# Kernel optimization log

Hardware: AMD Instinct MI355X
Metric: run time of the kernel (lower is better)

Reference implementation:

```python
import jax, jax.numpy as jnp
import numpy as np

# GeoTempScheduler default: init_temp=0.1, gamma=0.9, patience=1; at step 0 -> temp = 0.1
TEMP = 0.1

R, K, D, DLOW, B = 8, 10, 256, 10, 4096


def setup_inputs() -> dict:
    key = jax.random.key(0)
    k1, k2 = jax.random.split(key)
    x = jax.random.normal(k1, (B, D), dtype=jnp.float32)
    # reset_parameters: Us ~ N(0, 0.1/sqrt(D))
    Us = jax.random.normal(k2, (R, K, D, DLOW), dtype=jnp.float32) * (0.1 / np.sqrt(D))
    return {"x": x, "Us": Us}


def reference(x, Us):
    # encode: project data onto each (replicate, cluster) subspace basis
    # z: (r, k, B, d)
    z = jnp.einsum('bD,rkDd->rkbd', x, Us)
    # decode: x_ = z @ Us^T  -> (r, k, B, D)
    x_ = jnp.einsum('rkbd,rkDd->rkbD', z, Us)
    # l2-squared reconstruction loss, (r, k, B) -> permuted to (B, r, k)
    loss = 0.5 * jnp.sum((x_ - x) ** 2, axis=-1)
    assign_obj = jnp.transpose(loss, (2, 0, 1))  # (B, r, k)
    # set_assign uses detached objective (loss.data): temperature-scaled soft assignment
    c = jax.nn.softmax(-jax.lax.stop_gradient(assign_obj) / TEMP, axis=2)  # (B, r, k)
    # x_ * c.permute(1,2,0).unsqueeze(3), summed over clusters -> (r, B, D)
    out = jnp.einsum('rkbD,brk->rbD', x_, c)
    return out
```

## Files before the change

### kernel.cpp

```cpp
#include <hip/hip_runtime.h>
#include <math.h>

typedef unsigned short ushort_t;
typedef unsigned int uint32_tt;
typedef __attribute__((ext_vector_type(8))) short bf16x8;
typedef __attribute__((ext_vector_type(4))) float f32x4;

#define NR   8
#define NK   10
#define ND   256
#define NDL  10
#define NB   4096
#define NN   100
#define NP   112
#define NP2  128

#define WS_GP   0
#define WS_XB   32768
#define WS_U1   (32768 + 2097152)
#define WS_U2   (WS_U1 + 458752)
#define WS_NEED (WS_U2 + 524288)

__device__ __forceinline__ ushort_t f2bf(float f) {
    uint32_tt u = __float_as_uint(f);
    u = (u + 0x7FFF + ((u >> 16) & 1)) >> 16;
    return (ushort_t)u;
}

__global__ __launch_bounds__(256) void prep_kernel(const float* __restrict__ x,
                                                   const float* __restrict__ Us,
                                                   char* __restrict__ ws) {
    __shared__ float lu[ND * NDL];
    const int bid = blockIdx.x, tid = threadIdx.x;

    if (bid >= 80) {
        ushort_t* xb = (ushort_t*)(ws + WS_XB);
        const int base = (bid - 80) * 1024;
        #pragma unroll
        for (int v = 0; v < 4; ++v) {
            int i = base + v * 256 + tid;
            float4 vv = ((const float4*)x)[i];
            uint32_tt p0 = (uint32_tt)f2bf(vv.x) | ((uint32_tt)f2bf(vv.y) << 16);
            uint32_tt p1 = (uint32_tt)f2bf(vv.z) | ((uint32_tt)f2bf(vv.w) << 16);
            ((uint2*)xb)[i] = make_uint2(p0, p1);
        }
        return;
    }

    const int rk = bid;
    const int r  = rk / NK, k = rk - r * NK;
    const float* U = Us + (size_t)rk * ND * NDL;
    for (int i = tid; i < 640; i += 256)
        ((float4*)lu)[i] = ((const float4*)U)[i];
    __syncthreads();

    float* Gp = (float*)(ws + WS_GP);
    if (tid < NDL * NDL) {
        int d1 = tid / NDL, d2 = tid - d1 * NDL;
        float acc = 0.f;
        #pragma unroll 8
        for (int Di = 0; Di < ND; ++Di)
            acc += lu[Di * NDL + d1] * lu[Di * NDL + d2];
        Gp[(size_t)rk * 100 + tid] = (d1 == d2 ? 10.0f : 0.0f) - 5.0f * acc;
    }

    ushort_t* u1 = (ushort_t*)(ws + WS_U1);
    for (int p = tid; p < ND * NDL; p += 256) {
        int d = p >> 8, D = p & 255;
        u1[((size_t)r * NP + k * NDL + d) * ND + D] = f2bf(lu[D * NDL + d]);
    }

    ushort_t* u2 = (ushort_t*)(ws + WS_U2);
    {
        int D = tid;
        uint32_tt* dst = (uint32_tt*)(u2 + ((size_t)r * ND + D) * NP2 + k * NDL);
        const float* src = lu + D * NDL;
        #pragma unroll
        for (int j = 0; j < 5; ++j)
            dst[j] = (uint32_tt)f2bf(src[2 * j]) | ((uint32_tt)f2bf(src[2 * j + 1]) << 16);
    }

    if (k == NK - 1) {
        for (int p = tid; p < 12 * ND; p += 256) {
            int n = p >> 8, D = p & 255;
            u1[((size_t)r * NP + 100 + n) * ND + D] = 0;
        }
        uint32_tt* u2u = (uint32_tt*)u2;
        #pragma unroll
        for (int j = 0; j < 14; ++j)
            u2u[((size_t)r * ND + tid) * (NP2 / 2) + 50 + j] = 0;
    }
}

__global__ __launch_bounds__(256, 2) void ksub_mfma8(const char* __restrict__ ws,
                                                     float* __restrict__ out) {
    __shared__ __align__(16) char smem[37280];
    float*    zbuf = (float*)smem;
    ushort_t* wTb  = (ushort_t*)smem;
    float*    ot   = (float*)smem;
    float*    gp   = (float*)(smem + 33280);

    const int tid  = threadIdx.x;
    const int w    = tid >> 6;
    const int lane = tid & 63;
    const int c    = lane & 15;
    const int q    = lane >> 4;
    const int bid  = blockIdx.x;
    const int xcd  = bid & 7;
    const int idx  = bid >> 3;
    const int r    = idx & 7;
    const int b0   = (xcd * 16 + (idx >> 3)) * 32;
    const int bloc = (w & 1) * 16 + c;
    const int pair = w >> 1;

    const ushort_t* xb  = (const ushort_t*)(ws + WS_XB) + (size_t)(b0 + bloc) * ND + q * 8;
    const ushort_t* u1g = (const ushort_t*)(ws + WS_U1) + (size_t)r * NP * ND + c * ND + q * 8;
    const ushort_t* u2g = (const ushort_t*)(ws + WS_U2) + (size_t)r * ND * NP2 + c * NP2 + q * 8;
    const float*    gpg = (const float*)(ws + WS_GP) + (size_t)r * 1000;

    for (int i = tid; i < 1000; i += 256) gp[i] = gpg[i];

    bf16x8 xfr[8];
    #pragma unroll
    for (int Dc = 0; Dc < 8; ++Dc)
        xfr[Dc] = *(const bf16x8*)(xb + Dc * 32);

    f32x4 acc1[4];
    #pragma unroll
    for (int t = 0; t < 4; ++t) acc1[t] = (f32x4){0.f, 0.f, 0.f, 0.f};

    #pragma unroll
    for (int Dc = 0; Dc < 8; ++Dc) {
        bf16x8 a[4];
        #pragma unroll
        for (int tt = 0; tt < 4; ++tt) {
            int t = pair * 4 + tt;
            if (t < 7)
                a[tt] = *(const bf16x8*)(u1g + t * 16 * ND + Dc * 32);
        }
        #pragma unroll
        for (int tt = 0; tt < 4; ++tt) {
            int t = pair * 4 + tt;
            if (t < 7)
                acc1[tt] = __builtin_amdgcn_mfma_f32_16x16x32_bf16(a[tt], xfr[Dc], acc1[tt], 0, 0, 0);
        }
    }

    const int Dbase = pair * 128;
    bf16x8 a3[8];
    #pragma unroll
    for (int jj = 0; jj < 8; ++jj)
        a3[jj] = *(const bf16x8*)(u2g + (size_t)(Dbase + jj * 16) * NP2);

    #pragma unroll
    for (int tt = 0; tt < 4; ++tt) {
        int t = pair * 4 + tt;
        if (t < 7) {
            #pragma unroll
            for (int rg = 0; rg < 4; ++rg) {
                int n = t * 16 + q * 4 + rg;
                if (n < NN) zbuf[bloc * 100 + n] = acc1[tt][rg];
            }
        }
    }
    __syncthreads();

    const int bsm = tid >> 3;
    const int kq  = tid & 7;
    float zk[2][10], ee[2];
    {
        const float* zr = zbuf + bsm * 100;
        float L[2];
        #pragma unroll
        for (int jj = 0; jj < 2; ++jj) {
            int k = kq + 8 * jj;
            L[jj] = -1e30f;
            if (k < NK) {
                #pragma unroll
                for (int d = 0; d < 10; ++d) zk[jj][d] = zr[k * 10 + d];
                const float* g = gp + k * 100;
                float acc = 0.f;
                #pragma unroll
                for (int d1 = 0; d1 < 10; ++d1) {
                    float t2 = 0.f;
                    #pragma unroll
                    for (int d2 = 0; d2 < 10; ++d2) t2 += g[d1 * 10 + d2] * zk[jj][d2];
                    acc += t2 * zk[jj][d1];
                }
                L[jj] = acc;
            }
        }
        float m = fmaxf(L[0], L[1]);
        m = fmaxf(m, __shfl_xor(m, 1));
        m = fmaxf(m, __shfl_xor(m, 2));
        m = fmaxf(m, __shfl_xor(m, 4));
        float s = 0.f;
        #pragma unroll
        for (int jj = 0; jj < 2; ++jj) {
            ee[jj] = (kq + 8 * jj < NK) ? __expf(L[jj] - m) : 0.f;
            s += ee[jj];
        }
        s += __shfl_xor(s, 1);
        s += __shfl_xor(s, 2);
        s += __shfl_xor(s, 4);
        float inv = 1.0f / s;
        #pragma unroll
        for (int jj = 0; jj < 2; ++jj) ee[jj] *= inv;
    }
    __syncthreads();

    #pragma unroll
    for (int jj = 0; jj < 2; ++jj) {
        int k = kq + 8 * jj;
        if (k < NK) {
            #pragma unroll
            for (int d = 0; d < 10; ++d)
                wTb[bsm * 136 + k * 10 + d] = f2bf(ee[jj] * zk[jj][d]);
        }
    }
    {
        int row = tid >> 4, p = tid & 15;
        if (row < 32 && p < 14) ((uint32_tt*)wTb)[row * 68 + 50 + p] = 0;
        row = (tid + 256) >> 4;
        if (row < 32 && p < 14) ((uint32_tt*)wTb)[row * 68 + 50 + p] = 0;
    }
    __syncthreads();

    f32x4 acc3[8];
    #pragma unroll
    for (int t = 0; t < 8; ++t) acc3[t] = (f32x4){0.f, 0.f, 0.f, 0.f};

    #pragma unroll
    for (int nc = 0; nc < 4; ++nc) {
        bf16x8 bfr = *(const bf16x8*)(wTb + bloc * 136 + nc * 32 + q * 8);
        bf16x8 a[8];
        if (nc == 0) {
            #pragma unroll
            for (int jj = 0; jj < 8; ++jj) a[jj] = a3[jj];
        } else {
            #pragma unroll
            for (int jj = 0; jj < 8; ++jj)
                a[jj] = *(const bf16x8*)(u2g + (size_t)(Dbase + jj * 16) * NP2 + nc * 32);
        }
        #pragma unroll
        for (int jj = 0; jj < 8; ++jj)
            acc3[jj] = __builtin_amdgcn_mfma_f32_16x16x32_bf16(a[jj], bfr, acc3[jj], 0, 0, 0);
    }

    __syncthreads();
    #pragma unroll
    for (int jj = 0; jj < 8; ++jj)
        *(f32x4*)(ot + bloc * 260 + Dbase + jj * 16 + q * 4) = acc3[jj];
    __syncthreads();
    const size_t orow = (size_t)r * NB + b0;
    #pragma unroll
    for (int i = 0; i < 8; ++i) {
        int g4 = i * 256 + tid;
        int b  = g4 >> 6;
        int c4 = g4 & 63;
        f32x4 v = *(const f32x4*)(ot + b * 260 + c4 * 4);
        __builtin_nontemporal_store(v, (f32x4*)(out + (orow + b) * ND + c4 * 4));
    }
}

#define XS_S 68
#define US_S 132
#define ZB_S 104
#define WT_S 68
#define U2_S 68
#define OFF_WT 0
#define OFF_SH 6800
#define OFF_GP 13600
#define SMEM_F 14600

__global__ __launch_bounds__(128) void gram_kernel(const float* __restrict__ Us,
                                                   float* __restrict__ Gp) {
    int rk = blockIdx.x;
    const float* U = Us + (size_t)rk * ND * NDL;
    __shared__ float u[ND * NDL];
    for (int i = threadIdx.x; i < ND * NDL; i += blockDim.x) u[i] = U[i];
    __syncthreads();
    int e = threadIdx.x;
    if (e < NDL * NDL) {
        int d1 = e / NDL, d2 = e % NDL;
        float acc = 0.f;
        #pragma unroll 8
        for (int Di = 0; Di < ND; ++Di)
            acc += u[Di * NDL + d1] * u[Di * NDL + d2];
        Gp[(size_t)rk * (NDL * NDL) + e] = (d1 == d2 ? 10.0f : 0.0f) - 5.0f * acc;
    }
}

__global__ __launch_bounds__(256, 2) void ksub_fused(const float* __restrict__ x,
                                                     const float* __restrict__ Us,
                                                     const float* __restrict__ Gp,
                                                     float* __restrict__ out) {
    __shared__ float smemf[SMEM_F];
    float* wT   = smemf + OFF_WT;
    float* xsf  = smemf + OFF_SH;
    float* usf  = smemf + OFF_SH + 2176;
    float* zbuf = smemf + OFF_SH;
    float* u2   = smemf + OFF_SH;
    float* gp   = smemf + OFF_GP;

    const int tid = threadIdx.x;
    const int r   = blockIdx.y;
    const int b0  = blockIdx.x * 64;

    for (int i = tid; i < NK * NDL * NDL; i += 256)
        gp[i] = Gp[(size_t)r * (NK * NDL * NDL) + i];

    const int nt = tid & 15;
    const int bt = tid >> 4;
    float acc[4][8];
    #pragma unroll
    for (int j = 0; j < 4; ++j)
        #pragma unroll
        for (int i = 0; i < 8; ++i) acc[j][i] = 0.f;

    for (int cch = 0; cch < 8; ++cch) {
        __syncthreads();
        for (int i = tid; i < 512; i += 256) {
            int b = i >> 3, f = i & 7;
            float4 v = ((const float4*)(x + (size_t)(b0 + b) * ND))[cch * 8 + f];
            float* dst = xsf + (f * 4) * XS_S + b;
            dst[0] = v.x; dst[XS_S] = v.y; dst[2 * XS_S] = v.z; dst[3 * XS_S] = v.w;
        }
        for (int p = tid; p < 320; p += 256) {
            int k = p >> 5, Dl = p & 31;
            const float* g = Us + ((size_t)((r * NK + k) * ND) + cch * 32 + Dl) * NDL;
            float* dst = usf + Dl * US_S + k * NDL;
            #pragma unroll
            for (int d = 0; d < 10; ++d) dst[d] = g[d];
        }
        __syncthreads();
        #pragma unroll 4
        for (int Dl = 0; Dl < 32; ++Dl) {
            float4 xv = *(const float4*)(xsf + Dl * XS_S + bt * 4);
            float4 ua = *(const float4*)(usf + Dl * US_S + nt * 8);
            float4 ub = *(const float4*)(usf + Dl * US_S + nt * 8 + 4);
            float xa[4] = {xv.x, xv.y, xv.z, xv.w};
            float uu[8] = {ua.x, ua.y, ua.z, ua.w, ub.x, ub.y, ub.z, ub.w};
            #pragma unroll
            for (int j = 0; j < 4; ++j)
                #pragma unroll
                for (int i = 0; i < 8; ++i) acc[j][i] += xa[j] * uu[i];
        }
    }
    __syncthreads();
    if (nt < 12) {
        #pragma unroll
        for (int j = 0; j < 4; ++j) {
            float* zp = zbuf + (bt * 4 + j) * ZB_S + nt * 8;
            *(float4*)(zp)     = make_float4(acc[j][0], acc[j][1], acc[j][2], acc[j][3]);
            *(float4*)(zp + 4) = make_float4(acc[j][4], acc[j][5], acc[j][6], acc[j][7]);
        }
    } else if (nt == 12) {
        #pragma unroll
        for (int j = 0; j < 4; ++j) {
            float* zp = zbuf + (bt * 4 + j) * ZB_S + 96;
            *(float4*)(zp) = make_float4(acc[j][0], acc[j][1], acc[j][2], acc[j][3]);
        }
    }
    __syncthreads();
    if (tid < 64) {
        const int b_l = tid;
        const float* zrow = zbuf + b_l * ZB_S;
        float L[10];
        #pragma unroll
        for (int k = 0; k < NK; ++k) {
            float zkk[10];
            #pragma unroll
            for (int d = 0; d < 10; ++d) zkk[d] = zrow[k * 10 + d];
            const float* g = gp + k * 100;
            float a2 = 0.f;
            #pragma unroll
            for (int d1 = 0; d1 < 10; ++d1) {
                float t = 0.f;
                #pragma unroll
                for (int d2 = 0; d2 < 10; ++d2) t += g[d1 * 10 + d2] * zkk[d2];
                a2 += t * zkk[d1];
            }
            L[k] = a2;
        }
        float m = L[0];
        #pragma unroll
        for (int k = 1; k < NK; ++k) m = fmaxf(m, L[k]);
        float e[10], s = 0.f;
        #pragma unroll
        for (int k = 0; k < NK; ++k) { e[k] = __expf(L[k] - m); s += e[k]; }
        float inv = 1.0f / s;
        #pragma unroll
        for (int k = 0; k < NK; ++k) {
            float ck = e[k] * inv;
            #pragma unroll
            for (int d = 0; d < 10; ++d)
                wT[(k * 10 + d) * WT_S + b_l] = ck * zrow[k * 10 + d];
        }
    }
    const int Dt  = tid & 15;
    const int bt2 = tid >> 4;
    for (int c2 = 0; c2 < 4; ++c2) {
        __syncthreads();
        for (int p = tid; p < 640; p += 256) {
            int k = p >> 6, Dl = p & 63;
            const float* g = Us + ((size_t)((r * NK + k) * ND) + c2 * 64 + Dl) * NDL;
            float* dst = u2 + (k * NDL) * U2_S + Dl;
            #pragma unroll
            for (int d = 0; d < 10; ++d) dst[d * U2_S] = g[d];
        }
        __syncthreads();
        float o[4][4];
        #pragma unroll
        for (int j = 0; j < 4; ++j)
            #pragma unroll
            for (int i = 0; i < 4; ++i) o[j][i] = 0.f;
        #pragma unroll 4
        for (int n = 0; n < NN; ++n) {
            float4 wv = *(const float4*)(wT + n * WT_S + bt2 * 4);
            float4 uv = *(const float4*)(u2 + n * U2_S + Dt * 4);
            float wa[4] = {wv.x, wv.y, wv.z, wv.w};
            float ub[4] = {uv.x, uv.y, uv.z, uv.w};
            #pragma unroll
            for (int j = 0; j < 4; ++j)
                #pragma unroll
                for (int i = 0; i < 4; ++i) o[j][i] += wa[j] * ub[i];
        }
        #pragma unroll
        for (int j = 0; j < 4; ++j) {
            float* op = out + ((size_t)r * NB + b0 + bt2 * 4 + j) * ND + c2 * 64 + Dt * 4;
            *(float4*)op = make_float4(o[j][0], o[j][1], o[j][2], o[j][3]);
        }
    }
}

extern "C" void kernel_launch(void* const* d_in, const int* in_sizes, int n_in,
                              void* d_out, int out_size, void* d_ws, size_t ws_size,
                              hipStream_t stream) {
    const float* x  = (const float*)d_in[0];
    const float* Us = (const float*)d_in[1];
    float* out = (float*)d_out;

    if (ws_size >= (size_t)WS_NEED) {
        prep_kernel<<<dim3(336), 256, 0, stream>>>(x, Us, (char*)d_ws);
        ksub_mfma8<<<dim3(1024), 256, 0, stream>>>((const char*)d_ws, out);
    } else {
        gram_kernel<<<dim3(NR * NK), 128, 0, stream>>>(Us, (float*)d_ws);
        ksub_fused<<<dim3(NB / 64, NR), 256, 0, stream>>>(x, Us, (float*)d_ws, out);
    }
}
```

Before: 105.2 us.

## Split fused MFMA kernel into z/softmax and output GEMM kernels

The single fused kernel is split in two. The first computes z and the softmax weights and writes them as bf16 to an 8 MB global workspace. A second kernel reads those weights and runs the output GEMM, storing MFMA accumulators straight to global memory without staging through LDS. The x-to-bf16 conversion moves from the prep kernel into the first kernel, so prep launches only 80 blocks. This trades an extra launch and an extra round trip of the weights through global memory for lower LDS use, fewer barriers and possibly higher occupancy in each kernel.

```diff
diff --git a/kernel.cpp b/kernel.cpp
--- a/kernel.cpp
+++ b/kernel.cpp
@@ -16,10 +16,10 @@
 #define NP2  128
 
 #define WS_GP   0
-#define WS_XB   32768
-#define WS_U1   (32768 + 2097152)
+#define WS_U1   32768
 #define WS_U2   (WS_U1 + 458752)
-#define WS_NEED (WS_U2 + 524288)
+#define WS_W    (WS_U2 + 524288)
+#define WS_NEED (WS_W + 8388608)
 
 __device__ __forceinline__ ushort_t f2bf(float f) {
     uint32_tt u = __float_as_uint(f);
@@ -27,27 +27,11 @@
     return (ushort_t)u;
 }
 
-__global__ __launch_bounds__(256) void prep_kernel(const float* __restrict__ x,
-                                                   const float* __restrict__ Us,
+__global__ __launch_bounds__(256) void prep_kernel(const float* __restrict__ Us,
                                                    char* __restrict__ ws) {
     __shared__ float lu[ND * NDL];
-    const int bid = blockIdx.x, tid = threadIdx.x;
-
-    if (bid >= 80) {
-        ushort_t* xb = (ushort_t*)(ws + WS_XB);
-        const int base = (bid - 80) * 1024;
-        #pragma unroll
-        for (int v = 0; v < 4; ++v) {
-            int i = base + v * 256 + tid;
-            float4 vv = ((const float4*)x)[i];
-            uint32_tt p0 = (uint32_tt)f2bf(vv.x) | ((uint32_tt)f2bf(vv.y) << 16);
-            uint32_tt p1 = (uint32_tt)f2bf(vv.z) | ((uint32_tt)f2bf(vv.w) << 16);
-            ((uint2*)xb)[i] = make_uint2(p0, p1);
-        }
-        return;
-    }
-
-    const int rk = bid;
+    const int tid = threadIdx.x;
+    const int rk = blockIdx.x;
     const int r  = rk / NK, k = rk - r * NK;
     const float* U = Us + (size_t)rk * ND * NDL;
     for (int i = tid; i < 640; i += 256)
@@ -92,13 +76,12 @@
     }
 }
 
-__global__ __launch_bounds__(256, 2) void ksub_mfma8(const char* __restrict__ ws,
-                                                     float* __restrict__ out) {
-    __shared__ __align__(16) char smem[37280];
+__global__ __launch_bounds__(256) void zsoft_kernel(const float* __restrict__ x,
+                                                    char* __restrict__ ws) {
+    __shared__ __align__(16) char smem[16800];
     float*    zbuf = (float*)smem;
     ushort_t* wTb  = (ushort_t*)smem;
-    float*    ot   = (float*)smem;
-    float*    gp   = (float*)(smem + 33280);
+    float*    gp   = (float*)(smem + 12800);
 
     const int tid  = threadIdx.x;
     const int w    = tid >> 6;
@@ -113,24 +96,26 @@
     const int bloc = (w & 1) * 16 + c;
     const int pair = w >> 1;
 
-    const ushort_t* xb  = (const ushort_t*)(ws + WS_XB) + (size_t)(b0 + bloc) * ND + q * 8;
+    const float*    xg  = x + (size_t)(b0 + bloc) * ND + q * 8;
     const ushort_t* u1g = (const ushort_t*)(ws + WS_U1) + (size_t)r * NP * ND + c * ND + q * 8;
-    const ushort_t* u2g = (const ushort_t*)(ws + WS_U2) + (size_t)r * ND * NP2 + c * NP2 + q * 8;
     const float*    gpg = (const float*)(ws + WS_GP) + (size_t)r * 1000;
 
     for (int i = tid; i < 1000; i += 256) gp[i] = gpg[i];
 
-    bf16x8 xfr[8];
-    #pragma unroll
-    for (int Dc = 0; Dc < 8; ++Dc)
-        xfr[Dc] = *(const bf16x8*)(xb + Dc * 32);
-
     f32x4 acc1[4];
     #pragma unroll
     for (int t = 0; t < 4; ++t) acc1[t] = (f32x4){0.f, 0.f, 0.f, 0.f};
 
     #pragma unroll
     for (int Dc = 0; Dc < 8; ++Dc) {
+        float4 xa = *(const float4*)(xg + Dc * 32);
+        float4 xb4 = *(const float4*)(xg + Dc * 32 + 4);
+        bf16x8 xf;
+        xf[0] = (short)f2bf(xa.x);  xf[1] = (short)f2bf(xa.y);
+        xf[2] = (short)f2bf(xa.z);  xf[3] = (short)f2bf(xa.w);
+        xf[4] = (short)f2bf(xb4.x); xf[5] = (short)f2bf(xb4.y);
+        xf[6] = (short)f2bf(xb4.z); xf[7] = (short)f2bf(xb4.w);
+
         bf16x8 a[4];
         #pragma unroll
         for (int tt = 0; tt < 4; ++tt) {
@@ -142,15 +127,9 @@
         for (int tt = 0; tt < 4; ++tt) {
             int t = pair * 4 + tt;
             if (t < 7)
-                acc1[tt] = __builtin_amdgcn_mfma_f32_16x16x32_bf16(a[tt], xfr[Dc], acc1[tt], 0, 0, 0);
-        }
-    }
-
-    const int Dbase = pair * 128;
-    bf16x8 a3[8];
-    #pragma unroll
-    for (int jj = 0; jj < 8; ++jj)
-        a3[jj] = *(const bf16x8*)(u2g + (size_t)(Dbase + jj * 16) * NP2);
+                acc1[tt] = __builtin_amdgcn_mfma_f32_16x16x32_bf16(a[tt], xf, acc1[tt], 0, 0, 0);
+        }
+    }
 
     #pragma unroll
     for (int tt = 0; tt < 4; ++tt) {
@@ -226,41 +205,53 @@
     }
     __syncthreads();
 
-    f32x4 acc3[8];
-    #pragma unroll
-    for (int t = 0; t < 8; ++t) acc3[t] = (f32x4){0.f, 0.f, 0.f, 0.f};
+    uint32_tt* wgu = (uint32_tt*)(ws + WS_W + ((size_t)r * NB + b0) * (NP2 * 2));
+    const uint32_tt* wTu = (const uint32_tt*)wTb;
+    #pragma unroll
+    for (int i = tid; i < 2048; i += 256) {
+        int row = i >> 6, col = i & 63;
+        wgu[row * 64 + col] = wTu[row * 68 + col];
+    }
+}
+
+__global__ __launch_bounds__(256) void outgemm_kernel(const char* __restrict__ ws,
+                                                      float* __restrict__ out) {
+    const int tid  = threadIdx.x;
+    const int w    = tid >> 6;
+    const int lane = tid & 63;
+    const int c    = lane & 15;
+    const int q    = lane >> 4;
+    const int bid  = blockIdx.x;
+    const int xcd  = bid & 7;
+    const int idx  = bid >> 3;
+    const int r    = idx & 7;
+    const int b0   = (xcd * 16 + (idx >> 3)) * 32;
+    const int bloc = (w & 1) * 16 + c;
+    const int Dbase = (w >> 1) * 128;
+
+    const ushort_t* u2g = (const ushort_t*)(ws + WS_U2) + (size_t)r * ND * NP2 + c * NP2 + q * 8;
+    const ushort_t* wg  = (const ushort_t*)(ws + WS_W)  + ((size_t)r * NB + b0 + bloc) * NP2 + q * 8;
+
+    f32x4 acc[8];
+    #pragma unroll
+    for (int j = 0; j < 8; ++j) acc[j] = (f32x4){0.f, 0.f, 0.f, 0.f};
 
     #pragma unroll
     for (int nc = 0; nc < 4; ++nc) {
-        bf16x8 bfr = *(const bf16x8*)(wTb + bloc * 136 + nc * 32 + q * 8);
+        bf16x8 bfr = *(const bf16x8*)(wg + nc * 32);
         bf16x8 a[8];
-        if (nc == 0) {
-            #pragma unroll
-            for (int jj = 0; jj < 8; ++jj) a[jj] = a3[jj];
-        } else {
-            #pragma unroll
-            for (int jj = 0; jj < 8; ++jj)
-                a[jj] = *(const bf16x8*)(u2g + (size_t)(Dbase + jj * 16) * NP2 + nc * 32);
-        }
         #pragma unroll
         for (int jj = 0; jj < 8; ++jj)
-            acc3[jj] = __builtin_amdgcn_mfma_f32_16x16x32_bf16(a[jj], bfr, acc3[jj], 0, 0, 0);
-    }
-
-    __syncthreads();
+            a[jj] = *(const bf16x8*)(u2g + (size_t)(Dbase + jj * 16) * NP2 + nc * 32);
+        #pragma unroll
+        for (int jj = 0; jj < 8; ++jj)
+            acc[jj] = __builtin_amdgcn_mfma_f32_16x16x32_bf16(a[jj], bfr, acc[jj], 0, 0, 0);
+    }
+
+    const size_t orow = (size_t)r * NB + b0 + bloc;
     #pragma unroll
     for (int jj = 0; jj < 8; ++jj)
-        *(f32x4*)(ot + bloc * 260 + Dbase + jj * 16 + q * 4) = acc3[jj];
-    __syncthreads();
-    const size_t orow = (size_t)r * NB + b0;
-    #pragma unroll
-    for (int i = 0; i < 8; ++i) {
-        int g4 = i * 256 + tid;
-        int b  = g4 >> 6;
-        int c4 = g4 & 63;
-        f32x4 v = *(const f32x4*)(ot + b * 260 + c4 * 4);
-        __builtin_nontemporal_store(v, (f32x4*)(out + (orow + b) * ND + c4 * 4));
-    }
+        __builtin_nontemporal_store(acc[jj], (f32x4*)(out + orow * ND + Dbase + jj * 16 + q * 4));
 }
 
 #define XS_S 68
@@ -442,8 +433,9 @@
     float* out = (float*)d_out;
 
     if (ws_size >= (size_t)WS_NEED) {
-        prep_kernel<<<dim3(336), 256, 0, stream>>>(x, Us, (char*)d_ws);
-        ksub_mfma8<<<dim3(1024), 256, 0, stream>>>((const char*)d_ws, out);
+        prep_kernel<<<dim3(80), 256, 0, stream>>>(Us, (char*)d_ws);
+        zsoft_kernel<<<dim3(1024), 256, 0, stream>>>(x, (char*)d_ws);
+        outgemm_kernel<<<dim3(1024), 256, 0, stream>>>((const char*)d_ws, out);
     } else {
         gram_kernel<<<dim3(NR * NK), 128, 0, stream>>>(Us, (float*)d_ws);
         ksub_fused<<<dim3(NB / 64, NR), 256, 0, stream>>>(x, Us, (float*)d_ws, out);
```

Result: slower. 126.3 us (+20.0%).

## Fuse prep and main kernels into one launch with global flag sync

Applied to the files above, without the earlier changes.

Merges the prep and compute kernels into a single persistent-style launch of 512 blocks. The first 80 blocks compute the per-(r,k) Gram and bf16 basis data, then publish a per-rk magic value with a release store. Every block spin-waits on the ten flags for its replicate before processing two tiles. The separate x-to-bf16 pass is dropped; x is read as fp32 and converted in registers inside the MFMA loop. This saves a kernel launch and a workspace round-trip for x. In exchange it adds a spin-wait dependency that assumes the producer blocks get scheduled, and the magic-value flags are never reset between calls.

```diff
diff --git a/kernel.cpp b/kernel.cpp
--- a/kernel.cpp
+++ b/kernel.cpp
@@ -15,11 +15,11 @@
 #define NP   112
 #define NP2  128
 
-#define WS_GP   0
-#define WS_XB   32768
-#define WS_U1   (32768 + 2097152)
-#define WS_U2   (WS_U1 + 458752)
-#define WS_NEED (WS_U2 + 524288)
+#define WS_GP    0
+#define WS_U1    32768
+#define WS_U2    (32768 + 458752)
+#define WS_FLAGS (WS_U2 + 524288)
+#define WS_NEED  (WS_FLAGS + 320)
 
 __device__ __forceinline__ ushort_t f2bf(float f) {
     uint32_tt u = __float_as_uint(f);
@@ -27,28 +27,13 @@
     return (ushort_t)u;
 }
 
-__global__ __launch_bounds__(256) void prep_kernel(const float* __restrict__ x,
-                                                   const float* __restrict__ Us,
-                                                   char* __restrict__ ws) {
-    __shared__ float lu[ND * NDL];
-    const int bid = blockIdx.x, tid = threadIdx.x;
-
-    if (bid >= 80) {
-        ushort_t* xb = (ushort_t*)(ws + WS_XB);
-        const int base = (bid - 80) * 1024;
-        #pragma unroll
-        for (int v = 0; v < 4; ++v) {
-            int i = base + v * 256 + tid;
-            float4 vv = ((const float4*)x)[i];
-            uint32_tt p0 = (uint32_tt)f2bf(vv.x) | ((uint32_tt)f2bf(vv.y) << 16);
-            uint32_tt p1 = (uint32_tt)f2bf(vv.z) | ((uint32_tt)f2bf(vv.w) << 16);
-            ((uint2*)xb)[i] = make_uint2(p0, p1);
-        }
-        return;
-    }
-
-    const int rk = bid;
-    const int r  = rk / NK, k = rk - r * NK;
+__device__ __forceinline__ uint32_tt rk_magic(int rk) {
+    return 0x9E3779B9u * (uint32_tt)(rk + 1) ^ 0x5CA1AB1Eu;
+}
+
+__device__ __forceinline__ void prep_rk(int rk, int tid, const float* __restrict__ Us,
+                                        char* __restrict__ ws, float* lu) {
+    const int r = rk / NK, k = rk - r * NK;
     const float* U = Us + (size_t)rk * ND * NDL;
     for (int i = tid; i < 640; i += 256)
         ((float4*)lu)[i] = ((const float4*)U)[i];
@@ -92,20 +77,19 @@
     }
 }
 
-__global__ __launch_bounds__(256, 2) void ksub_mfma8(const char* __restrict__ ws,
-                                                     float* __restrict__ out) {
-    __shared__ __align__(16) char smem[37280];
+__device__ __forceinline__ void ksub_tile(int bid, int tid,
+                                          const float* __restrict__ x,
+                                          const char* __restrict__ ws,
+                                          float* __restrict__ out,
+                                          char* smem, const float* gp) {
     float*    zbuf = (float*)smem;
     ushort_t* wTb  = (ushort_t*)smem;
     float*    ot   = (float*)smem;
-    float*    gp   = (float*)(smem + 33280);
-
-    const int tid  = threadIdx.x;
+
     const int w    = tid >> 6;
     const int lane = tid & 63;
     const int c    = lane & 15;
     const int q    = lane >> 4;
-    const int bid  = blockIdx.x;
     const int xcd  = bid & 7;
     const int idx  = bid >> 3;
     const int r    = idx & 7;
@@ -113,17 +97,9 @@
     const int bloc = (w & 1) * 16 + c;
     const int pair = w >> 1;
 
-    const ushort_t* xb  = (const ushort_t*)(ws + WS_XB) + (size_t)(b0 + bloc) * ND + q * 8;
+    const float*    xg  = x + (size_t)(b0 + bloc) * ND + q * 8;
     const ushort_t* u1g = (const ushort_t*)(ws + WS_U1) + (size_t)r * NP * ND + c * ND + q * 8;
     const ushort_t* u2g = (const ushort_t*)(ws + WS_U2) + (size_t)r * ND * NP2 + c * NP2 + q * 8;
-    const float*    gpg = (const float*)(ws + WS_GP) + (size_t)r * 1000;
-
-    for (int i = tid; i < 1000; i += 256) gp[i] = gpg[i];
-
-    bf16x8 xfr[8];
-    #pragma unroll
-    for (int Dc = 0; Dc < 8; ++Dc)
-        xfr[Dc] = *(const bf16x8*)(xb + Dc * 32);
 
     f32x4 acc1[4];
     #pragma unroll
@@ -131,6 +107,14 @@
 
     #pragma unroll
     for (int Dc = 0; Dc < 8; ++Dc) {
+        float4 xa  = *(const float4*)(xg + Dc * 32);
+        float4 xb4 = *(const float4*)(xg + Dc * 32 + 4);
+        bf16x8 xf;
+        xf[0] = (short)f2bf(xa.x);  xf[1] = (short)f2bf(xa.y);
+        xf[2] = (short)f2bf(xa.z);  xf[3] = (short)f2bf(xa.w);
+        xf[4] = (short)f2bf(xb4.x); xf[5] = (short)f2bf(xb4.y);
+        xf[6] = (short)f2bf(xb4.z); xf[7] = (short)f2bf(xb4.w);
+
         bf16x8 a[4];
         #pragma unroll
         for (int tt = 0; tt < 4; ++tt) {
@@ -142,7 +126,7 @@
         for (int tt = 0; tt < 4; ++tt) {
             int t = pair * 4 + tt;
             if (t < 7)
-                acc1[tt] = __builtin_amdgcn_mfma_f32_16x16x32_bf16(a[tt], xfr[Dc], acc1[tt], 0, 0, 0);
+                acc1[tt] = __builtin_amdgcn_mfma_f32_16x16x32_bf16(a[tt], xf, acc1[tt], 0, 0, 0);
         }
     }
 
@@ -263,6 +247,52 @@
     }
 }
 
+__global__ __launch_bounds__(256, 2) void fused_one(const float* __restrict__ x,
+                                                    const float* __restrict__ Us,
+                                                    char* __restrict__ ws,
+                                                    float* __restrict__ out) {
+    __shared__ __align__(16) char smem[37280];
+    const int tid  = threadIdx.x;
+    const int bid0 = blockIdx.x;
+    uint32_tt* flg = (uint32_tt*)(ws + WS_FLAGS);
+
+    if (bid0 < 80) {
+        prep_rk(bid0, tid, Us, ws, (float*)smem);
+        __syncthreads();
+        if (tid == 0) {
+            __threadfence();
+            __hip_atomic_store(&flg[bid0], rk_magic(bid0),
+                               __ATOMIC_RELEASE, __HIP_MEMORY_SCOPE_AGENT);
+        }
+    }
+
+    const int r = (bid0 >> 3) & 7;
+
+    if (tid < 10) {
+        const int rk = r * 10 + tid;
+        const uint32_tt want = rk_magic(rk);
+        int guard = 0;
+        while (__hip_atomic_load(&flg[rk], __ATOMIC_ACQUIRE,
+                                 __HIP_MEMORY_SCOPE_AGENT) != want) {
+            __builtin_amdgcn_s_sleep(10);
+            if (++guard > (1 << 22)) break;
+        }
+    }
+    __syncthreads();
+
+    float* gp = (float*)(smem + 33280);
+    {
+        const float* gpg = (const float*)(ws + WS_GP) + (size_t)r * 1000;
+        for (int i = tid; i < 1000; i += 256) gp[i] = gpg[i];
+    }
+
+    #pragma unroll 1
+    for (int sub = 0; sub < 2; ++sub) {
+        __syncthreads();
+        ksub_tile(bid0 + sub * 512, tid, x, ws, out, smem, gp);
+    }
+}
+
 #define XS_S 68
 #define US_S 132
 #define ZB_S 104
@@ -442,8 +472,7 @@
     float* out = (float*)d_out;
 
     if (ws_size >= (size_t)WS_NEED) {
-        prep_kernel<<<dim3(336), 256, 0, stream>>>(x, Us, (char*)d_ws);
-        ksub_mfma8<<<dim3(1024), 256, 0, stream>>>((const char*)d_ws, out);
+        fused_one<<<dim3(512), 256, 0, stream>>>(x, Us, (char*)d_ws, out);
     } else {
         gram_kernel<<<dim3(NR * NK), 128, 0, stream>>>(Us, (float*)d_ws);
         ksub_fused<<<dim3(NB / 64, NR), 256, 0, stream>>>(x, Us, (float*)d_ws, out);
```

After: 148.4 us. 41.0% more time.
